# Kernel tuning notes

Hardware: AMD Instinct MI355X
Metric: run time of the kernel (lower is better)

The kernel has to match this reference:

```python
import jax, jax.numpy as jnp
import numpy as np

B, L = 16, 4096
D_IN, D_OUT, D_MODEL, N_LAYERS, N_STATE = 257, 257, 256, 4, 32  # 32 complex modes (= d_state 64 real)


def setup_inputs() -> dict:
    key = jax.random.key(0)
    ks = iter(jax.random.split(key, 24))
    nrm = lambda shape, s=0.02: jax.random.normal(next(ks), shape, jnp.float32) * s
    H, N = D_MODEL, N_STATE
    return {
        "x": jax.random.normal(next(ks), (B, L, D_IN, 2), jnp.float32),
        "enc_Wr": nrm((D_MODEL, D_IN)), "enc_Wi": nrm((D_MODEL, D_IN)),
        "enc_br": jnp.zeros((D_MODEL,), jnp.float32), "enc_bi": jnp.zeros((D_MODEL,), jnp.float32),
        # per layer (N_LAYERS) and per complex branch (2: real-branch S4D, imag-branch S4D)
        "s4_log_dt": jax.random.uniform(next(ks), (N_LAYERS, 2, H), jnp.float32,
                                        minval=float(np.log(0.001)), maxval=float(np.log(0.1))),
        "s4_log_A_real": jnp.broadcast_to(jnp.log(0.5 * jnp.ones((H, N), jnp.float32)), (N_LAYERS, 2, H, N)) + 0.0,
        "s4_A_imag": jnp.broadcast_to(jnp.pi * jnp.arange(N, dtype=jnp.float32), (N_LAYERS, 2, H, N)) + 0.0,
        "s4_C": jax.random.normal(next(ks), (N_LAYERS, 2, H, N, 2), jnp.float32) * (0.5 ** 0.5),
        "s4_D": jax.random.normal(next(ks), (N_LAYERS, 2, H), jnp.float32),
        "s4_Wout": nrm((N_LAYERS, 2, 2 * H, H)), "s4_bout": jnp.zeros((N_LAYERS, 2, 2 * H), jnp.float32),
        "ln_gamma": jnp.ones((N_LAYERS, 2, H), jnp.float32), "ln_beta": jnp.zeros((N_LAYERS, 2, H), jnp.float32),
        "dec_Wr": nrm((D_OUT, D_MODEL)), "dec_Wi": nrm((D_OUT, D_MODEL)),
        "dec_br": jnp.zeros((D_OUT,), jnp.float32), "dec_bi": jnp.zeros((D_OUT,), jnp.float32),
    }


def complex_linear(xr, xi, Wr, Wi, br, bi):
    yr = xr @ Wr.T - xi @ Wi.T + br
    yi = xr @ Wi.T + xi @ Wr.T + bi
    return yr, yi


def s4d_branch(u, log_dt, log_A_real, A_imag, C2, D, Wout, bout):
    """Standard S4D-minimal layer. u: (B, H, L) real."""
    Ln = u.shape[-1]
    dt = jnp.exp(log_dt)                            # (H,)
    A = -jnp.exp(log_A_real) + 1j * A_imag          # (H, N) complex
    C = C2[..., 0] + 1j * C2[..., 1]                # (H, N)
    dtA = A * dt[:, None]                           # (H, N)
    Cmod = C * (jnp.exp(dtA) - 1.0) / A
    vand = jnp.exp(dtA[..., None] * jnp.arange(Ln)) # (H, N, L)
    k = 2.0 * jnp.einsum('hn,hnl->hl', Cmod, vand).real  # (H, L)
    kf = jnp.fft.rfft(k, n=2 * Ln)
    uf = jnp.fft.rfft(u, n=2 * Ln)
    y = jnp.fft.irfft(uf * kf[None], n=2 * Ln)[..., :Ln]  # causal conv
    y = y + u * D[:, None]
    y = jax.nn.gelu(y, approximate=False)
    y = jnp.einsum('oh,bhl->bol', Wout, y) + bout[None, :, None]  # 1x1 conv to 2H
    a, g = jnp.split(y, 2, axis=1)                  # GLU over channel dim
    return a * jax.nn.sigmoid(g)


def layer_norm(x, gamma, beta):
    # x: (B, L, H), normalize over H (biased variance, like torch LayerNorm)
    mu = x.mean(-1, keepdims=True)
    var = x.var(-1, keepdims=True)
    return (x - mu) / jnp.sqrt(var + 1e-5) * gamma + beta


def reference(x, enc_Wr, enc_Wi, enc_br, enc_bi,
              s4_log_dt, s4_log_A_real, s4_A_imag, s4_C, s4_D, s4_Wout, s4_bout,
              ln_gamma, ln_beta, dec_Wr, dec_Wi, dec_br, dec_bi):
    xr, xi = complex_linear(x[..., 0], x[..., 1], enc_Wr, enc_Wi, enc_br, enc_bi)  # (B, L, H)
    xr = xr.swapaxes(-1, -2)  # (B, H, L)
    xi = xi.swapaxes(-1, -2)
    for l in range(N_LAYERS):
        sr = lambda u: s4d_branch(u, s4_log_dt[l, 0], s4_log_A_real[l, 0], s4_A_imag[l, 0],
                                  s4_C[l, 0], s4_D[l, 0], s4_Wout[l, 0], s4_bout[l, 0])
        si = lambda u: s4d_branch(u, s4_log_dt[l, 1], s4_log_A_real[l, 1], s4_A_imag[l, 1],
                                  s4_C[l, 1], s4_D[l, 1], s4_Wout[l, 1], s4_bout[l, 1])
        zr = sr(xr) - si(xi)
        zi = sr(xi) + si(xr)
        xr = xr + zr  # residual (dropout = identity)
        xi = xi + zi
        # post-norm over d_model (separate LN for real/imag parts)
        xr = layer_norm(xr.swapaxes(-1, -2), ln_gamma[l, 0], ln_beta[l, 0]).swapaxes(-1, -2)
        xi = layer_norm(xi.swapaxes(-1, -2), ln_gamma[l, 1], ln_beta[l, 1]).swapaxes(-1, -2)
    xr = xr.swapaxes(-1, -2)  # (B, L, H)
    xi = xi.swapaxes(-1, -2)
    yr, yi = complex_linear(xr, xi, dec_Wr, dec_Wi, dec_br, dec_bi)  # (B, L, D_OUT)
    return jnp.stack([yr, yi], axis=-1)
```

## Files before the change

kernel.cpp:

```cpp
#include <hip/hip_runtime.h>

typedef unsigned short ushort_t;
typedef unsigned int uint_t;
typedef __attribute__((ext_vector_type(8))) short short8;
typedef __attribute__((ext_vector_type(4))) float f32x4;

#define B_    16
#define L_    4096
#define H_    256
#define N_    32
#define DIN_  257
#define DOUT_ 257
#define NL_   4
#define Q_    128
#define NC_   32
#define BL_   (B_*L_)
#define NH_   (N_*H_)
#define PLANE_ 16777216
#define SSZ_  4194304

__device__ __forceinline__ float bfu(ushort_t u) {
    union { uint_t i; float f; } v; v.i = ((uint_t)u) << 16; return v.f;
}
__device__ __forceinline__ ushort_t f2bf(float f) {
    union { float f; uint_t i; } v; v.f = f;
    uint_t x = v.i;
    return (ushort_t)((x + 0x7FFFu + ((x >> 16) & 1u)) >> 16);
}
__device__ __forceinline__ uint2 pack4(float a, float b, float c, float d) {
    uint2 r;
    r.x = (uint_t)f2bf(a) | ((uint_t)f2bf(b) << 16);
    r.y = (uint_t)f2bf(c) | ((uint_t)f2bf(d) << 16);
    return r;
}
__device__ __forceinline__ float ldi(const void* p, size_t i, int f32) {
    return f32 ? ((const float*)p)[i] : bfu(((const ushort_t*)p)[i]);
}

__device__ __forceinline__ void gl16(const ushort_t* g, ushort_t* l) {
    __builtin_amdgcn_global_load_lds(
        (const __attribute__((address_space(1))) uint_t*)g,
        (__attribute__((address_space(3))) uint_t*)l, 16, 0, 0);
}

__device__ __forceinline__ uint4 ld8bf(const void* W, size_t eoff, int f32) {
    uint4 r;
    if (f32) {
        const float* p = (const float*)W + eoff;
        float4 a = *(const float4*)p;
        float4 b = *(const float4*)(p + 4);
        r.x = (uint_t)f2bf(a.x) | ((uint_t)f2bf(a.y) << 16);
        r.y = (uint_t)f2bf(a.z) | ((uint_t)f2bf(a.w) << 16);
        r.z = (uint_t)f2bf(b.x) | ((uint_t)f2bf(b.y) << 16);
        r.w = (uint_t)f2bf(b.z) | ((uint_t)f2bf(b.w) << 16);
    } else {
        r = *(const uint4*)((const ushort_t*)W + eoff);
    }
    return r;
}

__device__ __forceinline__ short8 negbf(short8 v) {
    short8 r;
#pragma unroll
    for (int i = 0; i < 8; ++i) r[i] = (short)(v[i] ^ (short)0x8000);
    return r;
}

#define MFMA16(a, b, c) __builtin_amdgcn_mfma_f32_16x16x32_bf16((a), (b), (c), 0, 0, 0)

__global__ void probe_kernel(const void* __restrict__ x, int* __restrict__ flag) {
    __shared__ int cnt;
    if (threadIdx.x == 0) cnt = 0;
    __syncthreads();
    uint_t w = ((const uint_t*)x)[threadIdx.x];
    float f = bfu((ushort_t)(w & 0xFFFF));
    float a = fabsf(f);
    if (a > 1e-5f && a < 100.f) atomicAdd(&cnt, 1);
    __syncthreads();
    if (threadIdx.x == 0) *flag = (cnt > 128) ? 0 : 1;
}

__global__ __launch_bounds__(256) void param_kernel(
        const void* __restrict__ log_dt, const void* __restrict__ lAr,
        const void* __restrict__ Aim, const void* __restrict__ C2,
        float* __restrict__ params, const int* __restrict__ dfl) {
    int f32 = *dfl;
    int idx = blockIdx.x * 256 + threadIdx.x;
    int h  = idx & (H_ - 1);
    int n  = (idx >> 8) & (N_ - 1);
    int lb = idx >> 13;
    float dt = expf(ldi(log_dt, lb * H_ + h, f32));
    size_t pin = (size_t)(lb * H_ + h) * N_ + n;
    float Ar = -expf(ldi(lAr, pin, f32));
    float Ai = ldi(Aim, pin, f32);
    float Cr = ldi(C2, pin * 2, f32), Ci = ldi(C2, pin * 2 + 1, f32);
    float dr = Ar * dt, di = Ai * dt;
    float e  = expf(dr);
    float wr = e * cosf(di), wi = e * sinf(di);
    float Er = wr - 1.0f, Ei = wi;
    float inv = 1.0f / (Ar * Ar + Ai * Ai);
    float Fr = (Er * Ar + Ei * Ai) * inv;
    float Fi = (Ei * Ar - Er * Ai) * inv;
    float ctr = 2.0f * (Cr * Fr - Ci * Fi);
    float cti = 2.0f * (Cr * Fi + Ci * Fr);
    float eq = expf((float)Q_ * dr);
    float ph = (float)Q_ * di;
    float wqr = eq * cosf(ph), wqi = eq * sinf(ph);
    float* pb = params + (size_t)lb * 6 * NH_;
    int o = n * H_ + h;
    pb[0 * NH_ + o] = wr;  pb[1 * NH_ + o] = wi;
    pb[2 * NH_ + o] = ctr; pb[3 * NH_ + o] = cti;
    pb[4 * NH_ + o] = wqr; pb[5 * NH_ + o] = wqi;
}

__global__ __launch_bounds__(256) void enc_gemm(
        const void* __restrict__ x, const void* __restrict__ Wr,
        const void* __restrict__ Wi, const void* __restrict__ br,
        const void* __restrict__ bi, ushort_t* __restrict__ xr,
        ushort_t* __restrict__ xi, const int* __restrict__ dfl) {
    __shared__ float Ar_s[16][64], Ai_s[16][64], Wr_s[16][64], Wi_s[16][64];
    int f32 = *dfl;
    int m0 = blockIdx.x * 64, n0 = blockIdx.y * 64;
    int tid = threadIdx.x;
    int ty = tid >> 4, tx = tid & 15;
    float accR[4][4] = {{0}}, accI[4][4] = {{0}};
    for (int k0 = 0; k0 < DIN_; k0 += 16) {
#pragma unroll
        for (int j = 0; j < 4; ++j) {
            int p = tid * 4 + j;
            int m = p >> 4, kk = p & 15;
            int k = k0 + kk;
            float r = 0.f, im = 0.f;
            if (k < DIN_) {
                size_t pi = (size_t)(m0 + m) * DIN_ + k;
                if (f32) {
                    float2 v = ((const float2*)x)[pi];
                    r = v.x; im = v.y;
                } else {
                    uint_t v = ((const uint_t*)x)[pi];
                    r  = bfu((ushort_t)(v & 0xFFFF));
                    im = bfu((ushort_t)(v >> 16));
                }
            }
            Ar_s[kk][m] = r; Ai_s[kk][m] = im;
        }
        {
            int n = tid >> 2, kpos = (tid & 3) * 4;
#pragma unroll
            for (int j = 0; j < 4; ++j) {
                int k = k0 + kpos + j;
                float wr_ = 0.f, wi_ = 0.f;
                if (k < DIN_) {
                    wr_ = ldi(Wr, (size_t)(n0 + n) * DIN_ + k, f32);
                    wi_ = ldi(Wi, (size_t)(n0 + n) * DIN_ + k, f32);
                }
                Wr_s[kpos + j][n] = wr_; Wi_s[kpos + j][n] = wi_;
            }
        }
        __syncthreads();
#pragma unroll
        for (int kk = 0; kk < 16; ++kk) {
            float ar[4], ai[4], ur[4], ui[4];
#pragma unroll
            for (int i = 0; i < 4; ++i) {
                ar[i] = Ar_s[kk][ty * 4 + i]; ai[i] = Ai_s[kk][ty * 4 + i];
                ur[i] = Wr_s[kk][tx * 4 + i]; ui[i] = Wi_s[kk][tx * 4 + i];
            }
#pragma unroll
            for (int i = 0; i < 4; ++i)
#pragma unroll
                for (int j = 0; j < 4; ++j) {
                    accR[i][j] = fmaf(ar[i], ur[j], fmaf(-ai[i], ui[j], accR[i][j]));
                    accI[i][j] = fmaf(ar[i], ui[j], fmaf( ai[i], ur[j], accI[i][j]));
                }
        }
        __syncthreads();
    }
    float bR[4], bI[4];
#pragma unroll
    for (int j = 0; j < 4; ++j) {
        bR[j] = ldi(br, n0 + tx * 4 + j, f32);
        bI[j] = ldi(bi, n0 + tx * 4 + j, f32);
    }
#pragma unroll
    for (int i = 0; i < 4; ++i) {
        size_t row = (size_t)(m0 + ty * 4 + i);
        size_t off = row * H_ + n0 + tx * 4;
        *(uint2*)(xr + off) = pack4(accR[i][0] + bR[0], accR[i][1] + bR[1],
                                    accR[i][2] + bR[2], accR[i][3] + bR[3]);
        *(uint2*)(xi + off) = pack4(accI[i][0] + bI[0], accI[i][1] + bI[1],
                                    accI[i][2] + bI[2], accI[i][3] + bI[3]);
    }
}

__global__ __launch_bounds__(256) void pass_a(
        const ushort_t* __restrict__ U, const float* __restrict__ P, ushort_t* __restrict__ S) {
    int c = blockIdx.x, b = blockIdx.y, h = threadIdx.x;
    float wr[N_], wi[N_], sr[N_], si[N_];
#pragma unroll
    for (int n = 0; n < N_; ++n) {
        wr[n] = P[n * H_ + h]; wi[n] = P[NH_ + n * H_ + h];
        sr[n] = 0.f; si[n] = 0.f;
    }
    const ushort_t* u = U + (size_t)(b * L_ + c * Q_) * H_ + h;
    float uvn = bfu(u[0]);
    for (int t = 0; t < Q_; ++t) {
        float uv = uvn;
        int tn = (t + 1 < Q_) ? t + 1 : t;
        uvn = bfu(u[(size_t)tn * H_]);
#pragma unroll
        for (int n = 0; n < N_; ++n) {
            float nr = fmaf(wr[n], sr[n], fmaf(-wi[n], si[n], uv));
            si[n] = fmaf(wr[n], si[n], wi[n] * sr[n]);
            sr[n] = nr;
        }
    }
    size_t o = (size_t)(b * NC_ + c) * N_ * H_ + h;
#pragma unroll
    for (int n = 0; n < N_; ++n) {
        S[o + n * H_] = f2bf(sr[n]);
        S[o + n * H_ + SSZ_] = f2bf(si[n]);
    }
}

__global__ __launch_bounds__(256) void pass_b(
        const float* __restrict__ P, ushort_t* __restrict__ S) {
    int n = blockIdx.x, b = blockIdx.y, h = threadIdx.x;
    float wqr = P[4 * NH_ + n * H_ + h], wqi = P[5 * NH_ + n * H_ + h];
    float Xr = 0.f, Xi = 0.f;
    for (int c = 0; c < NC_; ++c) {
        size_t idx = ((size_t)(b * NC_ + c) * N_ + n) * H_ + h;
        float lr = bfu(S[idx]), li = bfu(S[idx + SSZ_]);
        S[idx] = f2bf(Xr); S[idx + SSZ_] = f2bf(Xi);
        float nr = fmaf(wqr, Xr, fmaf(-wqi, Xi, lr));
        Xi = fmaf(wqr, Xi, fmaf(wqi, Xr, li));
        Xr = nr;
    }
}

__global__ __launch_bounds__(256) void pass_c(
        const ushort_t* __restrict__ U, const float* __restrict__ P,
        const ushort_t* __restrict__ S, const void* __restrict__ Dp, int doff,
        ushort_t* __restrict__ G, const int* __restrict__ dfl) {
    int f32 = *dfl;
    int c = blockIdx.x, b = blockIdx.y;
    int tid = threadIdx.x;
    int h = blockIdx.z * 128 + (tid >> 1);
    int nb = (tid & 1) * 16;
    float wr[16], wi[16], cr[16], ci[16], sr[16], si[16];
#pragma unroll
    for (int i = 0; i < 16; ++i) {
        int o = (nb + i) * H_ + h;
        wr[i] = P[o]; wi[i] = P[NH_ + o];
        cr[i] = P[2 * NH_ + o]; ci[i] = P[3 * NH_ + o];
    }
    size_t so = (size_t)(b * NC_ + c) * N_ * H_ + h;
#pragma unroll
    for (int i = 0; i < 16; ++i) {
        sr[i] = bfu(S[so + (nb + i) * H_]);
        si[i] = bfu(S[so + (nb + i) * H_ + SSZ_]);
    }
    float Dv = ldi(Dp, (size_t)doff + h, f32);
    const ushort_t* u = U + (size_t)(b * L_ + c * Q_) * H_ + h;
    ushort_t* g = G + (size_t)(b * L_ + c * Q_) * H_ + h;
    float uvn = bfu(u[0]);
    for (int t = 0; t < Q_; ++t) {
        float uv = uvn;
        int tn = (t + 1 < Q_) ? t + 1 : t;
        uvn = bfu(u[(size_t)tn * H_]);
        float a0 = 0.f, a1 = 0.f;
#pragma unroll
        for (int i = 0; i < 16; ++i) {
            float nr = fmaf(wr[i], sr[i], fmaf(-wi[i], si[i], uv));
            si[i] = fmaf(wr[i], si[i], wi[i] * sr[i]);
            sr[i] = nr;
            if (i & 1) a1 = fmaf(cr[i], sr[i], fmaf(-ci[i], si[i], a1));
            else       a0 = fmaf(cr[i], sr[i], fmaf(-ci[i], si[i], a0));
        }
        float acc = a0 + a1;
        acc += __shfl_xor(acc, 1, 64);
        float y = fmaf(Dv, uv, acc);
        float ge = 0.5f * y * (1.0f + erff(y * 0.70710678118654752f));
        if ((tid & 1) == 0) g[(size_t)t * H_] = f2bf(ge);
    }
}

__global__ __launch_bounds__(256) void wout_gemm(
        const ushort_t* __restrict__ Gb, const void* __restrict__ W, size_t woff,
        const void* __restrict__ bo, int boff, ushort_t* __restrict__ Z, int mode,
        const int* __restrict__ dfl) {
    __shared__ __align__(16) ushort_t As[8192];
    __shared__ __align__(16) ushort_t Bs[8192];
    int f32 = *dfl;
    int m0 = blockIdx.x * 128, n0 = blockIdx.y * 64;
    int tid = threadIdx.x;
    int w = tid >> 6, l = tid & 63;
    int rb = w * 32;
    int lr = l & 15, lk = (l >> 4) << 4;
    int lsw = (l & 7) << 4;
    int arow = tid >> 3;
    int acb  = ((tid & 7) << 4) ^ ((arow & 7) << 4);
    int brow = tid >> 1;
    int bhalf = (tid & 1) << 6;
    int bsw = (brow & 7) << 4;
    int wrow = (brow < 64) ? (n0 + brow) : (192 + n0 + brow);
    f32x4 z4 = {0.f, 0.f, 0.f, 0.f};
    f32x4 acc[2][8];
#pragma unroll
    for (int mi = 0; mi < 2; ++mi)
#pragma unroll
        for (int nj = 0; nj < 8; ++nj) acc[mi][nj] = z4;

    for (int k0 = 0; k0 < H_; k0 += 64) {
        if (k0) __syncthreads();
        {
            const ushort_t* src = Gb + (size_t)(m0 + arow) * H_ + k0 + (acb >> 1);
            ushort_t* dst = As + tid * 8;
#pragma unroll
            for (int ch = 0; ch < 4; ++ch)
                gl16(src + (size_t)ch * 32 * H_, dst + ch * 2048);
        }
        {
            size_t wb = woff + (size_t)wrow * H_ + k0;
            char* bp = (char*)Bs + brow * 128;
#pragma unroll
            for (int cc = 0; cc < 4; ++cc) {
                int cb = bhalf + cc * 16;
                uint4 v = ld8bf(W, wb + (cb >> 1), f32);
                *(uint4*)(bp + (cb ^ bsw)) = v;
            }
        }
        __syncthreads();
#pragma unroll
        for (int ks = 0; ks < 2; ++ks) {
            int off = (ks * 64 + lk) ^ lsw;
            short8 a0 = *(const short8*)((const char*)As + (rb + lr) * 128 + off);
            short8 a1 = *(const short8*)((const char*)As + (rb + 16 + lr) * 128 + off);
#pragma unroll
            for (int nj = 0; nj < 8; ++nj) {
                short8 bv = *(const short8*)((const char*)Bs + (nj * 16 + lr) * 128 + off);
                acc[0][nj] = MFMA16(a0, bv, acc[0][nj]);
                acc[1][nj] = MFMA16(a1, bv, acc[1][nj]);
            }
        }
    }
    float ba[4], bg[4];
#pragma unroll
    for (int nj = 0; nj < 4; ++nj) {
        ba[nj] = ldi(bo, (size_t)boff + n0 + nj * 16 + lr, f32);
        bg[nj] = ldi(bo, (size_t)boff + 256 + n0 + nj * 16 + lr, f32);
    }
#pragma unroll
    for (int mi = 0; mi < 2; ++mi)
#pragma unroll
        for (int nj = 0; nj < 4; ++nj)
#pragma unroll
            for (int r = 0; r < 4; ++r) {
                float av = acc[mi][nj][r] + ba[nj];
                float gv = acc[mi][nj + 4][r] + bg[nj];
                float s = av * (1.0f / (1.0f + expf(-gv)));
                int row = m0 + rb + mi * 16 + ((l >> 4) << 2) + r;
                size_t zo = (size_t)row * H_ + n0 + nj * 16 + lr;
                if (mode == 0)      Z[zo] = f2bf(s);
                else if (mode == 1) Z[zo] = f2bf(bfu(Z[zo]) + s);
                else                Z[zo] = f2bf(bfu(Z[zo]) - s);
            }
}

__global__ __launch_bounds__(256) void combine_ln(
        ushort_t* __restrict__ xr, ushort_t* __restrict__ xi,
        const ushort_t* __restrict__ zr, const ushort_t* __restrict__ zi,
        const void* __restrict__ gamma, const void* __restrict__ beta, int layer,
        const int* __restrict__ dfl) {
    __shared__ float red[4][4];
    int f32 = *dfl;
    int l = blockIdx.x, b = blockIdx.y, h = threadIdx.x;
    size_t row = (size_t)(b * L_ + l) * H_ + h;
    float vr = bfu(xr[row]) + bfu(zr[row]);
    float vi = bfu(xi[row]) + bfu(zi[row]);
    float s0 = vr, s1 = vr * vr, s2 = vi, s3 = vi * vi;
#pragma unroll
    for (int off = 32; off >= 1; off >>= 1) {
        s0 += __shfl_xor(s0, off, 64); s1 += __shfl_xor(s1, off, 64);
        s2 += __shfl_xor(s2, off, 64); s3 += __shfl_xor(s3, off, 64);
    }
    int wv = h >> 6;
    if ((h & 63) == 0) { red[wv][0] = s0; red[wv][1] = s1; red[wv][2] = s2; red[wv][3] = s3; }
    __syncthreads();
    float S0 = red[0][0] + red[1][0] + red[2][0] + red[3][0];
    float S1 = red[0][1] + red[1][1] + red[2][1] + red[3][1];
    float S2 = red[0][2] + red[1][2] + red[2][2] + red[3][2];
    float S3 = red[0][3] + red[1][3] + red[2][3] + red[3][3];
    const float invH = 1.0f / 256.0f;
    float mur = S0 * invH, varr = S1 * invH - mur * mur;
    float mui = S2 * invH, vari = S3 * invH - mui * mui;
    float gr = ldi(gamma, (size_t)(layer * 2 + 0) * H_ + h, f32);
    float br_ = ldi(beta, (size_t)(layer * 2 + 0) * H_ + h, f32);
    float gi = ldi(gamma, (size_t)(layer * 2 + 1) * H_ + h, f32);
    float bi_ = ldi(beta, (size_t)(layer * 2 + 1) * H_ + h, f32);
    xr[row] = f2bf((vr - mur) * rsqrtf(varr + 1e-5f) * gr + br_);
    xi[row] = f2bf((vi - mui) * rsqrtf(vari + 1e-5f) * gi + bi_);
}

__global__ __launch_bounds__(256) void dec_gemm(
        const ushort_t* __restrict__ xr, const ushort_t* __restrict__ xi,
        const void* __restrict__ Wr, const void* __restrict__ Wi,
        const void* __restrict__ br, const void* __restrict__ bi,
        void* __restrict__ out, const int* __restrict__ dfl) {
    __shared__ __align__(16) ushort_t Ars[8192];
    __shared__ __align__(16) ushort_t Ais[8192];
    __shared__ __align__(16) ushort_t Brs[4096];
    __shared__ __align__(16) ushort_t Bis[4096];
    int f32 = *dfl;
    int m0 = blockIdx.x * 128, n0 = blockIdx.y * 64;
    int tid = threadIdx.x;
    int w = tid >> 6, l = tid & 63;
    int rb = w * 32;
    int lr = l & 15, lk = (l >> 4) << 4, lsw = (l & 7) << 4;
    int arow = tid >> 3;
    int acb  = ((tid & 7) << 4) ^ ((arow & 7) << 4);
    int brow = tid >> 2;
    int bq   = (tid & 3) << 5;
    int bsw  = (brow & 7) << 4;
    int wrow = n0 + brow;
    bool bvalid = wrow < DOUT_;
    uint4 zz; zz.x = zz.y = zz.z = zz.w = 0u;
    f32x4 z4 = {0.f, 0.f, 0.f, 0.f};
    f32x4 aR[2][4], aI[2][4];
#pragma unroll
    for (int mi = 0; mi < 2; ++mi)
#pragma unroll
        for (int nj = 0; nj < 4; ++nj) { aR[mi][nj] = z4; aI[mi][nj] = z4; }

    for (int k0 = 0; k0 < H_; k0 += 64) {
        if (k0) __syncthreads();
        {
            size_t so = (size_t)(m0 + arow) * H_ + k0 + (acb >> 1);
            ushort_t* dr = Ars + tid * 8;
            ushort_t* di = Ais + tid * 8;
#pragma unroll
            for (int ch = 0; ch < 4; ++ch) {
                gl16(xr + so + (size_t)ch * 32 * H_, dr + ch * 2048);
                gl16(xi + so + (size_t)ch * 32 * H_, di + ch * 2048);
            }
        }
        {
            size_t wb = (size_t)wrow * H_ + k0 + (bq >> 1);
            char* pr_ = (char*)Brs + brow * 128;
            char* pi_ = (char*)Bis + brow * 128;
#pragma unroll
            for (int cc = 0; cc < 2; ++cc) {
                int cb = bq + cc * 16;
                uint4 vr = zz, vi = zz;
                if (bvalid) {
                    vr = ld8bf(Wr, wb + cc * 8, f32);
                    vi = ld8bf(Wi, wb + cc * 8, f32);
                }
                *(uint4*)(pr_ + (cb ^ bsw)) = vr;
                *(uint4*)(pi_ + (cb ^ bsw)) = vi;
            }
        }
        __syncthreads();
#pragma unroll
        for (int ks = 0; ks < 2; ++ks) {
            int off = (ks * 64 + lk) ^ lsw;
            short8 x0 = *(const short8*)((const char*)Ars + (rb + lr) * 128 + off);
            short8 x1 = *(const short8*)((const char*)Ars + (rb + 16 + lr) * 128 + off);
            short8 y0 = *(const short8*)((const char*)Ais + (rb + lr) * 128 + off);
            short8 y1 = *(const short8*)((const char*)Ais + (rb + 16 + lr) * 128 + off);
#pragma unroll
            for (int nj = 0; nj < 4; ++nj) {
                short8 wr_ = *(const short8*)((const char*)Brs + (nj * 16 + lr) * 128 + off);
                short8 wi_ = *(const short8*)((const char*)Bis + (nj * 16 + lr) * 128 + off);
                short8 wn = negbf(wi_);
                aR[0][nj] = MFMA16(x0, wr_, aR[0][nj]);
                aR[0][nj] = MFMA16(y0, wn,  aR[0][nj]);
                aR[1][nj] = MFMA16(x1, wr_, aR[1][nj]);
                aR[1][nj] = MFMA16(y1, wn,  aR[1][nj]);
                aI[0][nj] = MFMA16(x0, wi_, aI[0][nj]);
                aI[0][nj] = MFMA16(y0, wr_, aI[0][nj]);
                aI[1][nj] = MFMA16(x1, wi_, aI[1][nj]);
                aI[1][nj] = MFMA16(y1, wr_, aI[1][nj]);
            }
        }
    }
#pragma unroll
    for (int nj = 0; nj < 4; ++nj) {
        int col = n0 + nj * 16 + lr;
        if (col < DOUT_) {
            float bR = ldi(br, col, f32), bI = ldi(bi, col, f32);
#pragma unroll
            for (int mi = 0; mi < 2; ++mi)
#pragma unroll
                for (int r = 0; r < 4; ++r) {
                    int row = m0 + rb + mi * 16 + ((l >> 4) << 2) + r;
                    size_t pi = (size_t)row * DOUT_ + col;
                    float re = aR[mi][nj][r] + bR;
                    float im = aI[mi][nj][r] + bI;
                    if (f32) {
                        ((float2*)out)[pi] = make_float2(re, im);
                    } else {
                        ((uint_t*)out)[pi] = (uint_t)f2bf(re) | ((uint_t)f2bf(im) << 16);
                    }
                }
        }
    }
}

extern "C" void kernel_launch(void* const* d_in, const int* in_sizes, int n_in,
                              void* d_out, int out_size, void* d_ws, size_t ws_size,
                              hipStream_t stream) {
    const void* x      = d_in[0];
    const void* enc_Wr = d_in[1];
    const void* enc_Wi = d_in[2];
    const void* enc_br = d_in[3];
    const void* enc_bi = d_in[4];
    const void* log_dt = d_in[5];
    const void* lAr    = d_in[6];
    const void* Aim    = d_in[7];
    const void* C2     = d_in[8];
    const void* Dp     = d_in[9];
    const void* Wout   = d_in[10];
    const void* bout   = d_in[11];
    const void* gamma  = d_in[12];
    const void* beta   = d_in[13];
    const void* dec_Wr = d_in[14];
    const void* dec_Wi = d_in[15];
    const void* dec_br = d_in[16];
    const void* dec_bi = d_in[17];

    ushort_t* xr = (ushort_t*)d_ws;
    ushort_t* xi = xr + (size_t)PLANE_;
    ushort_t* gb = xi + (size_t)PLANE_;
    ushort_t* st = gb + (size_t)PLANE_;
    int*      fl = (int*)(st + (size_t)2 * SSZ_);
    float*    pr = (float*)(fl + 64);
    ushort_t* zr = (ushort_t*)d_out;
    ushort_t* zi = zr + (size_t)PLANE_;

    probe_kernel<<<1, 256, 0, stream>>>(x, fl);
    param_kernel<<<256, 256, 0, stream>>>(log_dt, lAr, Aim, C2, pr, fl);
    enc_gemm<<<dim3(BL_ / 64, H_ / 64), 256, 0, stream>>>(x, enc_Wr, enc_Wi, enc_br, enc_bi, xr, xi, fl);

    for (int l = 0; l < NL_; ++l) {
        struct App { int br; const ushort_t* U; ushort_t* Zt; int mode; };
        App apps[4] = {
            {0, xr, zr, 0},
            {1, xi, zr, 2},
            {0, xi, zi, 0},
            {1, xr, zi, 1},
        };
        for (int a = 0; a < 4; ++a) {
            const float* P = pr + (size_t)(l * 2 + apps[a].br) * 6 * NH_;
            pass_a<<<dim3(NC_, B_), 256, 0, stream>>>(apps[a].U, P, st);
            pass_b<<<dim3(N_, B_), 256, 0, stream>>>(P, st);
            pass_c<<<dim3(NC_, B_, 2), 256, 0, stream>>>(apps[a].U, P, st,
                    Dp, (l * 2 + apps[a].br) * H_, gb, fl);
            wout_gemm<<<dim3(BL_ / 128, H_ / 64), 256, 0, stream>>>(gb,
                    Wout, (size_t)(l * 2 + apps[a].br) * 512 * H_,
                    bout, (l * 2 + apps[a].br) * 512,
                    apps[a].Zt, apps[a].mode, fl);
        }
        combine_ln<<<dim3(L_, B_), 256, 0, stream>>>(xr, xi, zr, zi, gamma, beta, l, fl);
    }

    dec_gemm<<<dim3(BL_ / 128, (DOUT_ + 63) / 64), 256, 0, stream>>>(
            xr, xi, dec_Wr, dec_Wi, dec_br, dec_bi, d_out, fl);
}
```

Measured before the change: 4.976 ms.

## Move encoder complex GEMM onto bf16 MFMA with pre-packed interleaved weights

Replaces the scalar-FMA complex encoder GEMM with a bf16 MFMA kernel. The interleaved (re,im) input is treated as a real K=514 matrix, and a new pack kernel builds combined [Wr,-Wi] and [Wi,Wr] weight rows in the state scratch buffer. The first 512 K entries go through swizzled LDS tiles and MFMA, and the last complex element is handled in the epilogue with scalar FMAs. This targets the FP32 ALU cost of the encoder. It adds a packing launch, reuses scratch memory, and rounds activations to bf16, which costs some precision.

New measurement: 4.674 ms. -6.1%, faster.

```diff
diff --git a/kernel.cpp b/kernel.cpp
--- a/kernel.cpp
+++ b/kernel.cpp
@@ -18,6 +18,7 @@
 #define NH_   (N_*H_)
 #define PLANE_ 16777216
 #define SSZ_  4194304
+#define EPK_  520
 
 __device__ __forceinline__ float bfu(ushort_t u) {
     union { uint_t i; float f; } v; v.i = ((uint_t)u) << 16; return v.f;
@@ -55,6 +56,25 @@
         r.w = (uint_t)f2bf(b.z) | ((uint_t)f2bf(b.w) << 16);
     } else {
         r = *(const uint4*)((const ushort_t*)W + eoff);
+    }
+    return r;
+}
+
+__device__ __forceinline__ uint4 ld8r(const void* x, size_t eoff, int f32) {
+    uint4 r;
+    if (f32) {
+        const float* p = (const float*)x + eoff;
+        float2 a = *(const float2*)p;
+        float2 b = *(const float2*)(p + 2);
+        float2 c = *(const float2*)(p + 4);
+        float2 d = *(const float2*)(p + 6);
+        r.x = (uint_t)f2bf(a.x) | ((uint_t)f2bf(a.y) << 16);
+        r.y = (uint_t)f2bf(b.x) | ((uint_t)f2bf(b.y) << 16);
+        r.z = (uint_t)f2bf(c.x) | ((uint_t)f2bf(c.y) << 16);
+        r.w = (uint_t)f2bf(d.x) | ((uint_t)f2bf(d.y) << 16);
+    } else {
+        const uint_t* q = (const uint_t*)((const ushort_t*)x + eoff);
+        r.x = q[0]; r.y = q[1]; r.z = q[2]; r.w = q[3];
     }
     return r;
 }
@@ -113,83 +133,125 @@
     pb[4 * NH_ + o] = wqr; pb[5 * NH_ + o] = wqi;
 }
 
+__global__ __launch_bounds__(256) void pack_enc(
+        const void* __restrict__ Wr, const void* __restrict__ Wi,
+        ushort_t* __restrict__ Wp, const int* __restrict__ dfl) {
+    int f32 = *dfl;
+    int n = blockIdx.x;
+    for (int k = threadIdx.x; k < 260; k += 256) {
+        float wr = 0.f, wi = 0.f;
+        if (k < DIN_) {
+            wr = ldi(Wr, (size_t)n * DIN_ + k, f32);
+            wi = ldi(Wi, (size_t)n * DIN_ + k, f32);
+        }
+        Wp[(size_t)n * EPK_ + 2 * k]             = f2bf(wr);
+        Wp[(size_t)n * EPK_ + 2 * k + 1]         = f2bf(-wi);
+        Wp[(size_t)(256 + n) * EPK_ + 2 * k]     = f2bf(wi);
+        Wp[(size_t)(256 + n) * EPK_ + 2 * k + 1] = f2bf(wr);
+    }
+}
+
 __global__ __launch_bounds__(256) void enc_gemm(
-        const void* __restrict__ x, const void* __restrict__ Wr,
-        const void* __restrict__ Wi, const void* __restrict__ br,
-        const void* __restrict__ bi, ushort_t* __restrict__ xr,
-        ushort_t* __restrict__ xi, const int* __restrict__ dfl) {
-    __shared__ float Ar_s[16][64], Ai_s[16][64], Wr_s[16][64], Wi_s[16][64];
+        const void* __restrict__ x, const ushort_t* __restrict__ Wp,
+        const void* __restrict__ br, const void* __restrict__ bi,
+        ushort_t* __restrict__ xr, ushort_t* __restrict__ xi,
+        const int* __restrict__ dfl) {
+    __shared__ __align__(16) ushort_t As[8192];
+    __shared__ __align__(16) ushort_t Brs[4096];
+    __shared__ __align__(16) ushort_t Bis[4096];
     int f32 = *dfl;
-    int m0 = blockIdx.x * 64, n0 = blockIdx.y * 64;
+    int m0 = blockIdx.x * 128, n0 = blockIdx.y * 64;
     int tid = threadIdx.x;
-    int ty = tid >> 4, tx = tid & 15;
-    float accR[4][4] = {{0}}, accI[4][4] = {{0}};
-    for (int k0 = 0; k0 < DIN_; k0 += 16) {
-#pragma unroll
-        for (int j = 0; j < 4; ++j) {
-            int p = tid * 4 + j;
-            int m = p >> 4, kk = p & 15;
-            int k = k0 + kk;
-            float r = 0.f, im = 0.f;
-            if (k < DIN_) {
-                size_t pi = (size_t)(m0 + m) * DIN_ + k;
-                if (f32) {
-                    float2 v = ((const float2*)x)[pi];
-                    r = v.x; im = v.y;
-                } else {
-                    uint_t v = ((const uint_t*)x)[pi];
-                    r  = bfu((ushort_t)(v & 0xFFFF));
-                    im = bfu((ushort_t)(v >> 16));
-                }
-            }
-            Ar_s[kk][m] = r; Ai_s[kk][m] = im;
-        }
+    int w = tid >> 6, l = tid & 63;
+    int rb = w * 32;
+    int lr = l & 15, lk = (l >> 4) << 4, lsw = (l & 7) << 4;
+    int arow = tid >> 1;
+    int ahalf = (tid & 1) << 6;
+    int asw = (arow & 7) << 4;
+    int brow = tid >> 2;
+    int bq = (tid & 3) << 5;
+    int bsw = (brow & 7) << 4;
+    f32x4 z4 = {0.f, 0.f, 0.f, 0.f};
+    f32x4 aR[2][4], aI[2][4];
+#pragma unroll
+    for (int mi = 0; mi < 2; ++mi)
+#pragma unroll
+        for (int nj = 0; nj < 4; ++nj) { aR[mi][nj] = z4; aI[mi][nj] = z4; }
+
+    for (int k0 = 0; k0 < 512; k0 += 64) {
+        if (k0) __syncthreads();
         {
-            int n = tid >> 2, kpos = (tid & 3) * 4;
-#pragma unroll
-            for (int j = 0; j < 4; ++j) {
-                int k = k0 + kpos + j;
-                float wr_ = 0.f, wi_ = 0.f;
-                if (k < DIN_) {
-                    wr_ = ldi(Wr, (size_t)(n0 + n) * DIN_ + k, f32);
-                    wi_ = ldi(Wi, (size_t)(n0 + n) * DIN_ + k, f32);
-                }
-                Wr_s[kpos + j][n] = wr_; Wi_s[kpos + j][n] = wi_;
+            char* pa = (char*)As + arow * 128;
+            size_t xbase = (size_t)(m0 + arow) * 2 * DIN_ + k0;
+#pragma unroll
+            for (int cc = 0; cc < 4; ++cc) {
+                int cb = ahalf + cc * 16;
+                uint4 v = ld8r(x, xbase + (cb >> 1), f32);
+                *(uint4*)(pa + (cb ^ asw)) = v;
+            }
+        }
+        {
+            const ushort_t* wr_p = Wp + (size_t)(n0 + brow) * EPK_ + k0;
+            const ushort_t* wi_p = Wp + (size_t)(256 + n0 + brow) * EPK_ + k0;
+            char* pr_ = (char*)Brs + brow * 128;
+            char* pi_ = (char*)Bis + brow * 128;
+#pragma unroll
+            for (int cc = 0; cc < 2; ++cc) {
+                int cb = bq + cc * 16;
+                *(uint4*)(pr_ + (cb ^ bsw)) = *(const uint4*)(wr_p + (cb >> 1));
+                *(uint4*)(pi_ + (cb ^ bsw)) = *(const uint4*)(wi_p + (cb >> 1));
             }
         }
         __syncthreads();
 #pragma unroll
-        for (int kk = 0; kk < 16; ++kk) {
-            float ar[4], ai[4], ur[4], ui[4];
-#pragma unroll
-            for (int i = 0; i < 4; ++i) {
-                ar[i] = Ar_s[kk][ty * 4 + i]; ai[i] = Ai_s[kk][ty * 4 + i];
-                ur[i] = Wr_s[kk][tx * 4 + i]; ui[i] = Wi_s[kk][tx * 4 + i];
-            }
-#pragma unroll
-            for (int i = 0; i < 4; ++i)
-#pragma unroll
-                for (int j = 0; j < 4; ++j) {
-                    accR[i][j] = fmaf(ar[i], ur[j], fmaf(-ai[i], ui[j], accR[i][j]));
-                    accI[i][j] = fmaf(ar[i], ui[j], fmaf( ai[i], ur[j], accI[i][j]));
-                }
-        }
-        __syncthreads();
-    }
-    float bR[4], bI[4];
-#pragma unroll
-    for (int j = 0; j < 4; ++j) {
-        bR[j] = ldi(br, n0 + tx * 4 + j, f32);
-        bI[j] = ldi(bi, n0 + tx * 4 + j, f32);
-    }
-#pragma unroll
-    for (int i = 0; i < 4; ++i) {
-        size_t row = (size_t)(m0 + ty * 4 + i);
-        size_t off = row * H_ + n0 + tx * 4;
-        *(uint2*)(xr + off) = pack4(accR[i][0] + bR[0], accR[i][1] + bR[1],
-                                    accR[i][2] + bR[2], accR[i][3] + bR[3]);
-        *(uint2*)(xi + off) = pack4(accI[i][0] + bI[0], accI[i][1] + bI[1],
-                                    accI[i][2] + bI[2], accI[i][3] + bI[3]);
+        for (int ks = 0; ks < 2; ++ks) {
+            int off = (ks * 64 + lk) ^ lsw;
+            short8 a0 = *(const short8*)((const char*)As + (rb + lr) * 128 + off);
+            short8 a1 = *(const short8*)((const char*)As + (rb + 16 + lr) * 128 + off);
+#pragma unroll
+            for (int nj = 0; nj < 4; ++nj) {
+                short8 wr_ = *(const short8*)((const char*)Brs + (nj * 16 + lr) * 128 + off);
+                short8 wi_ = *(const short8*)((const char*)Bis + (nj * 16 + lr) * 128 + off);
+                aR[0][nj] = MFMA16(a0, wr_, aR[0][nj]);
+                aR[1][nj] = MFMA16(a1, wr_, aR[1][nj]);
+                aI[0][nj] = MFMA16(a0, wi_, aI[0][nj]);
+                aI[1][nj] = MFMA16(a1, wi_, aI[1][nj]);
+            }
+        }
+    }
+    float xre8[8], xim8[8];
+#pragma unroll
+    for (int mi = 0; mi < 2; ++mi)
+#pragma unroll
+        for (int r = 0; r < 4; ++r) {
+            int row = m0 + rb + mi * 16 + ((l >> 4) << 2) + r;
+            size_t pi = (size_t)row * DIN_ + 256;
+            float re, im;
+            if (f32) { float2 v = ((const float2*)x)[pi]; re = v.x; im = v.y; }
+            else { uint_t v = ((const uint_t*)x)[pi];
+                   re = bfu((ushort_t)(v & 0xFFFF)); im = bfu((ushort_t)(v >> 16)); }
+            xre8[mi * 4 + r] = re; xim8[mi * 4 + r] = im;
+        }
+#pragma unroll
+    for (int nj = 0; nj < 4; ++nj) {
+        int col = n0 + nj * 16 + lr;
+        float wRr = bfu(Wp[(size_t)col * EPK_ + 512]);
+        float wRi = bfu(Wp[(size_t)col * EPK_ + 513]);
+        float wIr = bfu(Wp[(size_t)(256 + col) * EPK_ + 512]);
+        float wIi = bfu(Wp[(size_t)(256 + col) * EPK_ + 513]);
+        float bR = ldi(br, col, f32), bI = ldi(bi, col, f32);
+#pragma unroll
+        for (int mi = 0; mi < 2; ++mi)
+#pragma unroll
+            for (int r = 0; r < 4; ++r) {
+                int row = m0 + rb + mi * 16 + ((l >> 4) << 2) + r;
+                int q = mi * 4 + r;
+                float re = aR[mi][nj][r] + xre8[q] * wRr + xim8[q] * wRi + bR;
+                float im = aI[mi][nj][r] + xre8[q] * wIr + xim8[q] * wIi + bI;
+                size_t off = (size_t)row * H_ + col;
+                xr[off] = f2bf(re);
+                xi[off] = f2bf(im);
+            }
     }
 }
 
@@ -537,10 +599,12 @@
     float*    pr = (float*)(fl + 64);
     ushort_t* zr = (ushort_t*)d_out;
     ushort_t* zi = zr + (size_t)PLANE_;
+    ushort_t* Wp = st;
 
     probe_kernel<<<1, 256, 0, stream>>>(x, fl);
     param_kernel<<<256, 256, 0, stream>>>(log_dt, lAr, Aim, C2, pr, fl);
-    enc_gemm<<<dim3(BL_ / 64, H_ / 64), 256, 0, stream>>>(x, enc_Wr, enc_Wi, enc_br, enc_bi, xr, xi, fl);
+    pack_enc<<<256, 256, 0, stream>>>(enc_Wr, enc_Wi, Wp, fl);
+    enc_gemm<<<dim3(BL_ / 128, H_ / 64), 256, 0, stream>>>(x, Wp, enc_br, enc_bi, xr, xi, fl);
 
     for (int l = 0; l < NL_; ++l) {
         struct App { int br; const ushort_t* U; ushort_t* Zt; int mode; };
```
